# Optimization experiments

Hardware: AMD Instinct MI355X
Metric: run time of the kernel (lower is better)

The kernel has to match this reference:

```python
import jax, jax.numpy as jnp
import numpy as np

FEATURE_LENGTH = 512
EMBEDDING_DIM = 128
NUM_EMBEDDINGS = 2048
BATCH = 8192


def setup_inputs() -> dict:
    key = jax.random.key(0)
    k1, k2 = jax.random.split(key)
    feature = jax.random.normal(k1, (BATCH, FEATURE_LENGTH), dtype=jnp.float32)
    W = jax.random.normal(k2, (NUM_EMBEDDINGS, EMBEDDING_DIM), dtype=jnp.float32)
    return {"feature": feature, "W": W}


def reference(feature, W):
    # vqlizationWithLoss: nearest-codebook lookup + straight-through VQ loss
    f = feature.reshape(-1, EMBEDDING_DIM)  # [N, d], N = BATCH * FEATURE_LENGTH / d
    # expanded L2 distances: ||f||^2 - 2 f W^T + ||W||^2 (same argmin as cdist^2)
    d2 = (jnp.sum(f * f, axis=1, keepdims=True)
          - 2.0 * jnp.einsum('nd,kd->nk', f, W)
          + jnp.sum(W * W, axis=1))  # [N, K]
    j = jnp.argmin(d2, axis=1)  # [N]
    W_j = W[j]  # [N, d]
    out = W_j.reshape(-1, FEATURE_LENGTH)  # [BATCH, featureLength]
    f_sg = jax.lax.stop_gradient(f)
    W_j_sg = jax.lax.stop_gradient(W_j)
    loss = (jnp.sum((f - W_j_sg) ** 2, axis=1)
            + 0.25 * jnp.sum((f_sg - W_j) ** 2, axis=1))  # [N]
    loss = loss.reshape(-1, FEATURE_LENGTH // EMBEDDING_DIM).mean(axis=1)  # [BATCH]
    return loss, out
```

## Files before the change

kernel.cpp:

```cpp
#include <hip/hip_runtime.h>

#define D        128
#define KCODES   2048
#define NROWS    32768
#define BATCH    8192

typedef _Float16 f16x8 __attribute__((ext_vector_type(8)));
typedef float    f32x4 __attribute__((ext_vector_type(4)));

#define MFMA16(a, b, c) __builtin_amdgcn_mfma_f32_16x16x32_f16((a), (b), (c), 0, 0, 0)
#define INV2048 4.8828125e-4f

static __device__ __forceinline__ void gload16(const void* g, void* l) {
    __builtin_amdgcn_global_load_lds(
        (const __attribute__((address_space(1))) unsigned int*)g,
        (__attribute__((address_space(3))) unsigned int*)l, 16, 0, 0);
}

static __device__ __forceinline__ float dppmin16(float s) {
    int t;
    t = __builtin_amdgcn_update_dpp(0, __float_as_int(s), 0x121, 0xf, 0xf, true);
    s = fminf(s, __int_as_float(t));
    t = __builtin_amdgcn_update_dpp(0, __float_as_int(s), 0x122, 0xf, 0xf, true);
    s = fminf(s, __int_as_float(t));
    t = __builtin_amdgcn_update_dpp(0, __float_as_int(s), 0x124, 0xf, 0xf, true);
    s = fminf(s, __int_as_float(t));
    t = __builtin_amdgcn_update_dpp(0, __float_as_int(s), 0x128, 0xf, 0xf, true);
    s = fminf(s, __int_as_float(t));
    return s;
}

__global__ void wconv_kernel(const float* __restrict__ W,
                             _Float16* __restrict__ whf, _Float16* __restrict__ wlf,
                             float* __restrict__ wnorm) {
    int gid = blockIdx.x * 256 + threadIdx.x;
    int n = gid >> 4, s = gid & 15;
    const float4* src = (const float4*)(W + (size_t)n * D + s * 8);
    float4 a = src[0], b = src[1];
    float va[8] = {a.x, a.y, a.z, a.w, b.x, b.y, b.z, b.w};
    f16x8 hi, lo;
    float ss = 0.0f;
#pragma unroll
    for (int j = 0; j < 8; ++j) {
        _Float16 h = (_Float16)va[j];
        hi[j] = h;
        lo[j] = (_Float16)((va[j] - (float)h) * 2048.0f);
        ss += va[j] * va[j];
    }
    size_t idx = ((size_t)((n >> 4) * 4 + (s >> 2)) * 64 + (s & 3) * 16 + (n & 15));
    ((f16x8*)whf)[idx] = hi;
    ((f16x8*)wlf)[idx] = lo;
#pragma unroll
    for (int m = 1; m <= 8; m <<= 1) ss += __shfl_xor(ss, m);
    if (s == 0) wnorm[n] = ss;
}

__global__ void fconv_kernel(const float* __restrict__ f,
                             _Float16* __restrict__ fhf, _Float16* __restrict__ flf) {
    int gid = blockIdx.x * 256 + threadIdx.x;
    int n = gid >> 4, s = gid & 15;
    const float4* src = (const float4*)(f + (size_t)n * D + s * 8);
    float4 a = src[0], b = src[1];
    float va[8] = {a.x, a.y, a.z, a.w, b.x, b.y, b.z, b.w};
    f16x8 hi, lo;
#pragma unroll
    for (int j = 0; j < 8; ++j) {
        float x = -2.0f * va[j];
        _Float16 h = (_Float16)x;
        hi[j] = h;
        lo[j] = (_Float16)((x - (float)h) * 2048.0f);
    }
    size_t idx = ((size_t)((n >> 4) * 4 + (s >> 2)) * 64 + (s & 3) * 16 + (n & 15));
    ((f16x8*)fhf)[idx] = hi;
    ((f16x8*)flf)[idx] = lo;
}

extern "C" __global__ void __launch_bounds__(512)
__attribute__((amdgpu_flat_work_group_size(512, 512)))
__attribute__((amdgpu_waves_per_eu(2, 2)))
vq_argmin(const _Float16* __restrict__ fhf, const _Float16* __restrict__ flf,
          const _Float16* __restrict__ whf, const _Float16* __restrict__ wlf,
          const float* __restrict__ wnorm,
          float* __restrict__ bsp, int* __restrict__ bcp) {
    extern __shared__ unsigned char lds[];

    const int b   = blockIdx.x;
    const int cb  = b & 3;
    const int rg  = b >> 2;
    const int tid = threadIdx.x;
    const int w   = tid >> 6, l = tid & 63;
    const int l15 = l & 15, lq = l >> 4;

    const char* fhB = (const char*)fhf + (size_t)rg * 131072;
    const char* flB = (const char*)flf + (size_t)rg * 131072;

#define STAGE(c) {                                                          \
        unsigned char* dB = lds + ((c) & 1) * 65536;                        \
        const char* sh = fhB + (size_t)(c) * 32768;                         \
        const char* sl = flB + (size_t)(c) * 32768;                         \
        gload16(sh + tid * 16,         dB + tid * 16);                      \
        gload16(sh + 8192  + tid * 16, dB + 8192  + tid * 16);              \
        gload16(sh + 16384 + tid * 16, dB + 16384 + tid * 16);              \
        gload16(sh + 24576 + tid * 16, dB + 24576 + tid * 16);              \
        gload16(sl + tid * 16,         dB + 32768 + tid * 16);              \
        gload16(sl + 8192  + tid * 16, dB + 40960 + tid * 16);              \
        gload16(sl + 16384 + tid * 16, dB + 49152 + tid * 16);              \
        gload16(sl + 24576 + tid * 16, dB + 57344 + tid * 16);              \
    }

    STAGE(0);

    f16x8 wh[4][4], wl[4][4];
    {
        const f16x8* whv = (const f16x8*)whf;
        const f16x8* wlv = (const f16x8*)wlf;
        const int n0 = cb * 32 + w * 4;
#pragma unroll
        for (int ct = 0; ct < 4; ++ct)
#pragma unroll
            for (int ks = 0; ks < 4; ++ks) {
                size_t idx = (size_t)((n0 + ct) * 4 + ks) * 64 + l;
                wh[ct][ks] = whv[idx];
                wl[ct][ks] = wlv[idx];
            }
    }
    float wv[4];
    unsigned mv[4];
#pragma unroll
    for (int ct = 0; ct < 4; ++ct) {
        wv[ct] = wnorm[cb * 512 + w * 64 + ct * 16 + l15];
        mv[ct] = (unsigned)(ct << 4) | (unsigned)l15;
    }

    __syncthreads();

    float* mrg = (float*)(lds + 131072);

#pragma unroll 1
    for (int c = 0; c < 4; ++c) {
        if (c < 3) STAGE(c + 1);
        const unsigned char* wb = lds + (c & 1) * 65536;

#pragma unroll 2
        for (int tl = 0; tl < 8; ++tl) {
            f16x8 fhk[4], flk[4];
#pragma unroll
            for (int ks = 0; ks < 4; ++ks) {
                fhk[ks] = *(const f16x8*)(wb + ((tl * 4 + ks) << 10) + l * 16);
                flk[ks] = *(const f16x8*)(wb + 32768 + ((tl * 4 + ks) << 10) + l * 16);
            }

            f32x4 accC[4], accH[4];
#pragma unroll
            for (int ct = 0; ct < 4; ++ct)
#pragma unroll
                for (int r = 0; r < 4; ++r) { accC[ct][r] = 0.0f; accH[ct][r] = wv[ct]; }

#pragma unroll
            for (int ks = 0; ks < 4; ++ks) {
                __builtin_amdgcn_s_setprio(1);
#pragma unroll
                for (int ct = 0; ct < 4; ++ct)
                    accC[ct] = MFMA16(fhk[ks], wl[ct][ks], accC[ct]);
#pragma unroll
                for (int ct = 0; ct < 4; ++ct)
                    accH[ct] = MFMA16(fhk[ks], wh[ct][ks], accH[ct]);
#pragma unroll
                for (int ct = 0; ct < 4; ++ct)
                    accC[ct] = MFMA16(flk[ks], wh[ct][ks], accC[ct]);
                __builtin_amdgcn_s_setprio(0);
            }

            float bestR[4] = {3.4e38f, 3.4e38f, 3.4e38f, 3.4e38f};
#pragma unroll
            for (int ct = 0; ct < 4; ++ct)
#pragma unroll
                for (int r = 0; r < 4; ++r) {
                    float s = fmaf(accC[ct][r], INV2048, accH[ct][r]);
                    unsigned pk = (__float_as_uint(s) & 0xFFFFFFC0u) | mv[ct];
                    bestR[r] = fminf(bestR[r], __uint_as_float(pk));
                }
#pragma unroll
            for (int r = 0; r < 4; ++r) bestR[r] = dppmin16(bestR[r]);

            if (l15 == 0) {
                f32x4 v;
                v[0] = bestR[0]; v[1] = bestR[1]; v[2] = bestR[2]; v[3] = bestR[3];
                *(f32x4*)(mrg + w * 512 + c * 128 + tl * 16 + lq * 4) = v;
            }
        }
        asm volatile("s_waitcnt vmcnt(0)" ::: "memory");
        __builtin_amdgcn_s_barrier();
        asm volatile("" ::: "memory");
    }
#undef STAGE

    __syncthreads();
    {
        int row = tid;
        float s = mrg[row];
        int wBest = 0;
#pragma unroll
        for (int ww = 1; ww < 8; ++ww) {
            float s2 = mrg[ww * 512 + row];
            if (s2 < s) { s = s2; wBest = ww; }
        }
        unsigned bits = __float_as_uint(s);
        int code = cb * 512 + wBest * 64 + (int)((bits >> 4) & 3u) * 16 + (int)(bits & 15u);
        bsp[(size_t)cb * NROWS + rg * 512 + row] = s;
        bcp[(size_t)cb * NROWS + rg * 512 + row] = code;
    }
}

__global__ void gather_kernel(const float* __restrict__ f, const float* __restrict__ W,
                              const float* __restrict__ bsp, const int* __restrict__ bcp,
                              float* __restrict__ loss, float* __restrict__ outv) {
    int b  = blockIdx.x;
    int wv = threadIdx.x >> 6;
    int l  = threadIdx.x & 63;
    int n  = b * 4 + wv;
    float s; int c;
    if (l < 4) { s = bsp[(size_t)l * NROWS + n]; c = bcp[(size_t)l * NROWS + n]; }
    else       { s = 3.4e38f; c = 0x7FFFFFFF; }
#pragma unroll
    for (int msk = 1; msk <= 2; msk <<= 1) {
        float s2 = __shfl_xor(s, msk);
        int   c2 = __shfl_xor(c, msk);
        if (s2 < s || (s2 == s && c2 < c)) { s = s2; c = c2; }
    }
    int j = __shfl(c, 0);
    float2 fv = reinterpret_cast<const float2*>(f + (size_t)n * D)[l];
    float2 wj = reinterpret_cast<const float2*>(W + (size_t)j * D)[l];
    reinterpret_cast<float2*>(outv + (size_t)n * D)[l] = wj;
    float dx = fv.x - wj.x, dy = fv.y - wj.y;
    float ls = dx * dx + dy * dy;
#pragma unroll
    for (int off = 32; off; off >>= 1) ls += __shfl_down(ls, off);
    __shared__ float lsm[4];
    if (l == 0) lsm[wv] = ls;
    __syncthreads();
    if (threadIdx.x == 0)
        loss[b] = 1.25f * 0.25f * (lsm[0] + lsm[1] + lsm[2] + lsm[3]);
}

extern "C" void kernel_launch(void* const* d_in, const int* in_sizes, int n_in,
                              void* d_out, int out_size, void* d_ws, size_t ws_size,
                              hipStream_t stream) {
    const float* f = (const float*)d_in[0];
    const float* W = (const float*)d_in[1];

    float* loss = (float*)d_out;
    float* outv = (float*)d_out + BATCH;

    _Float16* fhf = (_Float16*)outv;
    _Float16* flf = (_Float16*)((char*)outv + 8388608);

    float*    wnorm = (float*)d_ws;
    _Float16* whf   = (_Float16*)((char*)d_ws + 8192);
    _Float16* wlf   = (_Float16*)((char*)d_ws + 532480);
    float*    bsp   = (float*)((char*)d_ws + 1056768);
    int*      bcp   = (int*)((char*)d_ws + 1581056);

    wconv_kernel<<<KCODES * 16 / 256, 256, 0, stream>>>(W, whf, wlf, wnorm);
    fconv_kernel<<<NROWS * 16 / 256, 256, 0, stream>>>(f, fhf, flf);

    hipLaunchKernelGGL(vq_argmin, dim3(256), dim3(512), 147456, stream,
                       fhf, flf, whf, wlf, wnorm, bsp, bcp);

    gather_kernel<<<BATCH, 256, 0, stream>>>(f, W, bsp, bcp, loss, outv);
}
```

Measured before the change: 66.99 us.

## Halve rows per argmin block and compute loss from norms plus min distance

Each argmin block now handles 256 rows instead of 512, giving 512 blocks with half the LDS staging. The aim is better occupancy and load balance across the 256 CUs. The gather kernel no longer rereads the feature rows. It computes loss as ||f||^2 plus the minimum expanded distance, using per-row norms that fconv now produces. This drops a full feature read, but the loss now rests on the fp16-split distance value rather than an exact fp32 difference, which may cost some accuracy.

```diff
diff --git a/kernel.cpp b/kernel.cpp
--- a/kernel.cpp
+++ b/kernel.cpp
@@ -56,15 +56,18 @@
 }
 
 __global__ void fconv_kernel(const float* __restrict__ f,
-                             _Float16* __restrict__ fhf, _Float16* __restrict__ flf) {
+                             _Float16* __restrict__ fhf, _Float16* __restrict__ flf,
+                             float* __restrict__ fnorm) {
     int gid = blockIdx.x * 256 + threadIdx.x;
     int n = gid >> 4, s = gid & 15;
     const float4* src = (const float4*)(f + (size_t)n * D + s * 8);
     float4 a = src[0], b = src[1];
     float va[8] = {a.x, a.y, a.z, a.w, b.x, b.y, b.z, b.w};
     f16x8 hi, lo;
+    float ss = 0.0f;
 #pragma unroll
     for (int j = 0; j < 8; ++j) {
+        ss += va[j] * va[j];
         float x = -2.0f * va[j];
         _Float16 h = (_Float16)x;
         hi[j] = h;
@@ -73,6 +76,9 @@
     size_t idx = ((size_t)((n >> 4) * 4 + (s >> 2)) * 64 + (s & 3) * 16 + (n & 15));
     ((f16x8*)fhf)[idx] = hi;
     ((f16x8*)flf)[idx] = lo;
+#pragma unroll
+    for (int m = 1; m <= 8; m <<= 1) ss += __shfl_xor(ss, m);
+    if (s == 0) fnorm[n] = ss;
 }
 
 extern "C" __global__ void __launch_bounds__(512)
@@ -91,21 +97,17 @@
     const int w   = tid >> 6, l = tid & 63;
     const int l15 = l & 15, lq = l >> 4;
 
-    const char* fhB = (const char*)fhf + (size_t)rg * 131072;
-    const char* flB = (const char*)flf + (size_t)rg * 131072;
+    const char* fhB = (const char*)fhf + (size_t)rg * 65536;
+    const char* flB = (const char*)flf + (size_t)rg * 65536;
 
 #define STAGE(c) {                                                          \
-        unsigned char* dB = lds + ((c) & 1) * 65536;                        \
-        const char* sh = fhB + (size_t)(c) * 32768;                         \
-        const char* sl = flB + (size_t)(c) * 32768;                         \
-        gload16(sh + tid * 16,         dB + tid * 16);                      \
-        gload16(sh + 8192  + tid * 16, dB + 8192  + tid * 16);              \
-        gload16(sh + 16384 + tid * 16, dB + 16384 + tid * 16);              \
-        gload16(sh + 24576 + tid * 16, dB + 24576 + tid * 16);              \
-        gload16(sl + tid * 16,         dB + 32768 + tid * 16);              \
-        gload16(sl + 8192  + tid * 16, dB + 40960 + tid * 16);              \
-        gload16(sl + 16384 + tid * 16, dB + 49152 + tid * 16);              \
-        gload16(sl + 24576 + tid * 16, dB + 57344 + tid * 16);              \
+        unsigned char* dB = lds + ((c) & 1) * 32768;                        \
+        const char* sh = fhB + (size_t)(c) * 16384;                         \
+        const char* sl = flB + (size_t)(c) * 16384;                         \
+        gload16(sh + tid * 16,        dB + tid * 16);                       \
+        gload16(sh + 8192 + tid * 16, dB + 8192 + tid * 16);                \
+        gload16(sl + tid * 16,        dB + 16384 + tid * 16);               \
+        gload16(sl + 8192 + tid * 16, dB + 24576 + tid * 16);               \
     }
 
     STAGE(0);
@@ -134,20 +136,20 @@
 
     __syncthreads();
 
-    float* mrg = (float*)(lds + 131072);
+    float* mrg = (float*)(lds + 65536);
 
 #pragma unroll 1
     for (int c = 0; c < 4; ++c) {
         if (c < 3) STAGE(c + 1);
-        const unsigned char* wb = lds + (c & 1) * 65536;
+        const unsigned char* wb = lds + (c & 1) * 32768;
 
 #pragma unroll 2
-        for (int tl = 0; tl < 8; ++tl) {
+        for (int tl = 0; tl < 4; ++tl) {
             f16x8 fhk[4], flk[4];
 #pragma unroll
             for (int ks = 0; ks < 4; ++ks) {
                 fhk[ks] = *(const f16x8*)(wb + ((tl * 4 + ks) << 10) + l * 16);
-                flk[ks] = *(const f16x8*)(wb + 32768 + ((tl * 4 + ks) << 10) + l * 16);
+                flk[ks] = *(const f16x8*)(wb + 16384 + ((tl * 4 + ks) << 10) + l * 16);
             }
 
             f32x4 accC[4], accH[4];
@@ -186,7 +188,7 @@
             if (l15 == 0) {
                 f32x4 v;
                 v[0] = bestR[0]; v[1] = bestR[1]; v[2] = bestR[2]; v[3] = bestR[3];
-                *(f32x4*)(mrg + w * 512 + c * 128 + tl * 16 + lq * 4) = v;
+                *(f32x4*)(mrg + w * 256 + c * 64 + tl * 16 + lq * 4) = v;
             }
         }
         asm volatile("s_waitcnt vmcnt(0)" ::: "memory");
@@ -196,23 +198,24 @@
 #undef STAGE
 
     __syncthreads();
-    {
+    if (tid < 256) {
         int row = tid;
         float s = mrg[row];
         int wBest = 0;
 #pragma unroll
         for (int ww = 1; ww < 8; ++ww) {
-            float s2 = mrg[ww * 512 + row];
+            float s2 = mrg[ww * 256 + row];
             if (s2 < s) { s = s2; wBest = ww; }
         }
         unsigned bits = __float_as_uint(s);
         int code = cb * 512 + wBest * 64 + (int)((bits >> 4) & 3u) * 16 + (int)(bits & 15u);
-        bsp[(size_t)cb * NROWS + rg * 512 + row] = s;
-        bcp[(size_t)cb * NROWS + rg * 512 + row] = code;
-    }
-}
-
-__global__ void gather_kernel(const float* __restrict__ f, const float* __restrict__ W,
+        bsp[(size_t)cb * NROWS + rg * 256 + row] = s;
+        bcp[(size_t)cb * NROWS + rg * 256 + row] = code;
+    }
+}
+
+__global__ void gather_kernel(const float* __restrict__ W,
+                              const float* __restrict__ fnorm,
                               const float* __restrict__ bsp, const int* __restrict__ bcp,
                               float* __restrict__ loss, float* __restrict__ outv) {
     int b  = blockIdx.x;
@@ -229,18 +232,14 @@
         if (s2 < s || (s2 == s && c2 < c)) { s = s2; c = c2; }
     }
     int j = __shfl(c, 0);
-    float2 fv = reinterpret_cast<const float2*>(f + (size_t)n * D)[l];
+    float smin = __shfl(s, 0);
     float2 wj = reinterpret_cast<const float2*>(W + (size_t)j * D)[l];
     reinterpret_cast<float2*>(outv + (size_t)n * D)[l] = wj;
-    float dx = fv.x - wj.x, dy = fv.y - wj.y;
-    float ls = dx * dx + dy * dy;
-#pragma unroll
-    for (int off = 32; off; off >>= 1) ls += __shfl_down(ls, off);
     __shared__ float lsm[4];
-    if (l == 0) lsm[wv] = ls;
+    if (l == 0) lsm[wv] = smin + fnorm[n];
     __syncthreads();
     if (threadIdx.x == 0)
-        loss[b] = 1.25f * 0.25f * (lsm[0] + lsm[1] + lsm[2] + lsm[3]);
+        loss[b] = 0.3125f * (lsm[0] + lsm[1] + lsm[2] + lsm[3]);
 }
 
 extern "C" void kernel_launch(void* const* d_in, const int* in_sizes, int n_in,
@@ -260,12 +259,13 @@
     _Float16* wlf   = (_Float16*)((char*)d_ws + 532480);
     float*    bsp   = (float*)((char*)d_ws + 1056768);
     int*      bcp   = (int*)((char*)d_ws + 1581056);
+    float*    fnorm = (float*)((char*)d_ws + 2105344);
 
     wconv_kernel<<<KCODES * 16 / 256, 256, 0, stream>>>(W, whf, wlf, wnorm);
-    fconv_kernel<<<NROWS * 16 / 256, 256, 0, stream>>>(f, fhf, flf);
-
-    hipLaunchKernelGGL(vq_argmin, dim3(256), dim3(512), 147456, stream,
+    fconv_kernel<<<NROWS * 16 / 256, 256, 0, stream>>>(f, fhf, flf, fnorm);
+
+    hipLaunchKernelGGL(vq_argmin, dim3(512), dim3(512), 73728, stream,
                        fhf, flf, whf, wlf, wnorm, bsp, bcp);
 
-    gather_kernel<<<BATCH, 256, 0, stream>>>(f, W, bsp, bcp, loss, outv);
-}
+    gather_kernel<<<BATCH, 256, 0, stream>>>(W, fnorm, bsp, bcp, loss, outv);
+}
```

New measurement: 67.91 us. Within noise of the previous version (+1.4%).
